# Performance work log

Hardware: AMD Instinct MI355X
Metric: run time of the kernel (lower is better)

## Reference

```python
import jax, jax.numpy as jnp
import numpy as np

B, S, H, A, F, NCATE, VOCAB, EMB, NCONT = 64, 1024, 512, 256, 2048, 4, 1000, 64, 4


def _layernorm(x, g, b, eps=1e-5):
    m = jnp.mean(x, axis=-1, keepdims=True)
    v = jnp.mean((x - m) ** 2, axis=-1, keepdims=True)
    return (x - m) * jax.lax.rsqrt(v + eps) * g + b


def _positional_encoding(seq_len, d, base=10000.0):
    pos = jnp.arange(seq_len, dtype=jnp.float32)[:, None]
    i = jnp.arange(0, d, 2, dtype=jnp.float32)[None, :]
    ang = pos / jnp.power(base, i / d)
    pe = jnp.zeros((seq_len, d), dtype=jnp.float32)
    pe = pe.at[:, 0::2].set(jnp.sin(ang))
    pe = pe.at[:, 1::2].set(jnp.cos(ang))
    return pe


def setup_inputs() -> dict:
    key = jax.random.key(0)
    ks = jax.random.split(key, 24)
    s = lambda i, shape, fan: jax.random.normal(ks[i], shape, jnp.float32) / np.sqrt(fan)
    inp = {
        'cate_x': jax.random.randint(ks[0], (B, S, NCATE), 0, VOCAB, jnp.int32),
        'cont_x': jax.random.normal(ks[1], (B, S, NCONT), jnp.float32),
        'mask': (jax.random.uniform(ks[2], (B, S)) < 0.9).astype(jnp.float32),
        'targets': jax.random.uniform(ks[3], (B, S), jnp.float32),
        'E_cate': s(4, (NCATE, VOCAB, EMB), EMB),
        'W_proj': s(5, (NCATE * EMB + NCONT, H), NCATE * EMB + NCONT),
        'WQ1': s(6, (H, A), H), 'WK1': s(7, (H, A), H), 'WV1': s(8, (H, A), H),
        'WQ2': s(9, (H, A), H), 'WK2': s(10, (H, A), H), 'WV2': s(11, (H, A), H),
        'W0': s(12, (2 * A, H), 2 * A),
        'ln1_g': jnp.ones((H,), jnp.float32), 'ln1_b': jnp.zeros((H,), jnp.float32),
        'Wf1': s(13, (H, F), H), 'bf1': jnp.zeros((F,), jnp.float32),
        'Wf2': s(14, (F, H), F), 'bf2': jnp.zeros((H,), jnp.float32),
        'ln2_g': jnp.ones((H,), jnp.float32), 'ln2_b': jnp.zeros((H,), jnp.float32),
        'Wfin': s(15, (H, 1), H), 'bfin': jnp.zeros((1,), jnp.float32),
    }
    return inp


def _attn_branch(x, WQ, WK, WV, mask_bias):
    Q = x @ WQ  # [B,S,A]
    K = x @ WK
    V = x @ WV
    scores = jnp.einsum('bsa,bta->bst', Q, K) / np.sqrt(A)
    scores = scores + mask_bias  # additive key-mask [B,1,S]
    return jnp.einsum('bst,bta->bsa', jax.nn.softmax(scores, axis=-1), V)


def reference(cate_x, cont_x, mask, targets, E_cate, W_proj, WQ1, WK1, WV1,
              WQ2, WK2, WV2, W0, ln1_g, ln1_b, Wf1, bf1, Wf2, bf2, ln2_g,
              ln2_b, Wfin, bfin):
    # embedding: per-feature lookup, concat with continuous, project to hidden
    emb = jax.vmap(lambda tab, idx: tab[idx], in_axes=(0, 2), out_axes=2)(E_cate, cate_x)
    emb = emb.reshape(B, S, NCATE * EMB)
    x = jnp.concatenate([emb, cont_x], axis=-1) @ W_proj  # [B,S,H]
    x = x + _positional_encoding(S, H)[None]
    mask_bias = (mask * 1e6 - 1e6)[:, None, :]  # [B,1,S]
    z1 = _attn_branch(x, WQ1, WK1, WV1, mask_bias)
    z2 = _attn_branch(x, WQ2, WK2, WV2, mask_bias)
    z = jnp.concatenate([z1, z2], axis=-1) @ W0
    z = _layernorm(x + z, ln1_g, ln1_b)
    fz = jax.nn.relu(z @ Wf1 + bf1) @ Wf2 + bf2
    z3 = _layernorm(z + fz, ln2_g, ln2_b)
    out = (z3 @ Wfin + bfin).squeeze(-1)  # [B,S]
    return out
```

## Files before the change

kernel.cpp:

```cpp
#include <hip/hip_runtime.h>

typedef unsigned short ushort_t;
typedef unsigned int uint32;
typedef float f32x4 __attribute__((ext_vector_type(4)));
typedef short bf16x8 __attribute__((ext_vector_type(8)));

__device__ __forceinline__ float bf2f(short u) {
  union { uint32 u32; float f; } cv;
  cv.u32 = ((uint32)(ushort_t)u) << 16;
  return cv.f;
}
__device__ __forceinline__ ushort_t f2bf(float f) {
  union { float f; uint32 u; } cv; cv.f = f;
  return (ushort_t)((cv.u + 0x7fffu + ((cv.u >> 16) & 1u)) >> 16);
}
__device__ __forceinline__ uint32 pack2bf(float lo, float hi) {
  return (uint32)f2bf(lo) | ((uint32)f2bf(hi) << 16);
}
__device__ __forceinline__ f32x4 mfma16(bf16x8 a, bf16x8 b, f32x4 c) {
  return __builtin_amdgcn_mfma_f32_16x16x32_bf16(a, b, c, 0, 0, 0);
}
__device__ __forceinline__ void gld_lds16(const ushort_t* g, ushort_t* l) {
  __builtin_amdgcn_global_load_lds(
      (const __attribute__((address_space(1))) void*)g,
      (__attribute__((address_space(3))) void*)l, 16, 0, 0);
}

struct TPtrs {
  const float* s[9];
  ushort_t* d[9];
};
__global__ __launch_bounds__(256)
void transpose_all(TPtrs p) {
  const int id = blockIdx.x;
  const float* S;
  ushort_t* D;
  int K, N, lt;
  if (id < 768) {
    const int wsel = id >> 7;
    lt = id & 127; S = p.s[wsel]; D = p.d[wsel]; K = 512; N = 256;
  } else if (id < 1024) {
    lt = id - 768; S = p.s[6]; D = p.d[6]; K = 512; N = 512;
  } else if (id < 2048) {
    lt = id - 1024; S = p.s[7]; D = p.d[7]; K = 512; N = 2048;
  } else {
    lt = id - 2048; S = p.s[8]; D = p.d[8]; K = 2048; N = 512;
  }
  const int ntn = N >> 5;
  const int k0 = (lt / ntn) * 32, n0 = (lt % ntn) * 32;
  __shared__ float sm[32][33];
  const int tx = threadIdx.x & 31, ty = threadIdx.x >> 5;
#pragma unroll
  for (int i = 0; i < 4; ++i)
    sm[ty + i * 8][tx] = S[(size_t)(k0 + ty + i * 8) * N + n0 + tx];
  __syncthreads();
#pragma unroll
  for (int i = 0; i < 4; ++i)
    D[(size_t)(n0 + ty + i * 8) * K + k0 + tx] = f2bf(sm[tx][ty + i * 8]);
}

__global__ __launch_bounds__(256)
void ep_kernel(const float* __restrict__ E, const float* __restrict__ Wp,
               ushort_t* __restrict__ EP) {
  const int cv = blockIdx.x;
  const int c = cv / 1000;
  __shared__ float se[64];
  if (threadIdx.x < 64) se[threadIdx.x] = E[(size_t)cv * 64 + threadIdx.x];
  __syncthreads();
  const float* wrow = Wp + (size_t)c * 64 * 512;
  for (int h = threadIdx.x; h < 512; h += 256) {
    float acc = 0.f;
#pragma unroll
    for (int e = 0; e < 64; ++e) acc += se[e] * wrow[(size_t)e * 512 + h];
    EP[(size_t)cv * 512 + h] = f2bf(acc);
  }
}

__global__ __launch_bounds__(256)
void pe_kernel(float* __restrict__ PE) {
  const int id = blockIdx.x * 256 + threadIdx.x;
  const int s = id >> 8, i = id & 255;
  const float ang = (float)s * exp2f(-(float)i * (13.287712379549449f / 256.0f));
  PE[(size_t)s * 512 + 2 * i] = sinf(ang);
  PE[(size_t)s * 512 + 2 * i + 1] = cosf(ang);
}

__global__ __launch_bounds__(256)
void x_kernel(const int* __restrict__ cate, const float* __restrict__ cont,
              const float* __restrict__ Wp, const ushort_t* __restrict__ EP,
              const float* __restrict__ PE, ushort_t* __restrict__ X) {
  const int tid = threadIdx.x;
  const size_t r = (size_t)blockIdx.x * 4 + (tid >> 6);
  const int lane = tid & 63;
  const int h0 = lane * 8;
  const int s = (int)(r & 1023);
  float acc[8];
  const float4 p0 = *(const float4*)(PE + (size_t)s * 512 + h0);
  const float4 p1 = *(const float4*)(PE + (size_t)s * 512 + h0 + 4);
  acc[0] = p0.x; acc[1] = p0.y; acc[2] = p0.z; acc[3] = p0.w;
  acc[4] = p1.x; acc[5] = p1.y; acc[6] = p1.z; acc[7] = p1.w;
#pragma unroll
  for (int c = 0; c < 4; ++c) {
    const int idx = cate[r * 4 + c];
    const bf16x8 e8 = *(const bf16x8*)(EP + ((size_t)(c * 1000 + idx)) * 512 + h0);
#pragma unroll
    for (int k = 0; k < 8; ++k) acc[k] += bf2f(e8[k]);
  }
#pragma unroll
  for (int j = 0; j < 4; ++j) {
    const float cj = cont[r * 4 + j];
    const float4 w0 = *(const float4*)(Wp + (size_t)(256 + j) * 512 + h0);
    const float4 w1 = *(const float4*)(Wp + (size_t)(256 + j) * 512 + h0 + 4);
    acc[0] += cj * w0.x; acc[1] += cj * w0.y; acc[2] += cj * w0.z; acc[3] += cj * w0.w;
    acc[4] += cj * w1.x; acc[5] += cj * w1.y; acc[6] += cj * w1.z; acc[7] += cj * w1.w;
  }
  bf16x8 ov;
#pragma unroll
  for (int k = 0; k < 8; ++k) ov[k] = (short)f2bf(acc[k]);
  *(bf16x8*)(X + r * 512 + h0) = ov;
}

template <int EPI, bool TSTORE>
__global__ __launch_bounds__(256, 3)
void gemm_bt(const ushort_t* __restrict__ A, const ushort_t* __restrict__ BT,
             ushort_t* __restrict__ C, const float* __restrict__ bias, int N, int K) {
  __shared__ __align__(16) ushort_t sA[128 * 64];
  __shared__ __align__(16) ushort_t sB[128 * 64];
  const int tid = threadIdx.x;
  const int lane = tid & 63;
  const int wid = tid >> 6;
  const int l15 = lane & 15, l4 = lane >> 4;
  const int wr = (wid >> 1) * 64, wc = (wid & 1) * 64;
  const size_t rowA0 = (size_t)blockIdx.x * 128;
  const size_t rowB0 = (size_t)blockIdx.y * 128;

  f32x4 acc[4][4] = {};

  for (int kt = 0; kt < K; kt += 64) {
#pragma unroll
    for (int it = 0; it < 4; ++it) {
      const int L = it * 256 + tid;
      const int row = L >> 3;
      const int c = (L & 7) ^ (row & 7);
      gld_lds16(A + (rowA0 + row) * K + kt + c * 8, sA + (size_t)L * 8);
      gld_lds16(BT + (rowB0 + row) * K + kt + c * 8, sB + (size_t)L * 8);
    }
    __syncthreads();
#pragma unroll
    for (int kk = 0; kk < 2; ++kk) {
      bf16x8 af[4], bfr[4];
#pragma unroll
      for (int mi = 0; mi < 4; ++mi) {
        const int row = wr + mi * 16 + l15;
        const int c = (kk * 4 + l4) ^ (row & 7);
        af[mi] = *(const bf16x8*)(sA + row * 64 + c * 8);
      }
#pragma unroll
      for (int ni = 0; ni < 4; ++ni) {
        const int row = wc + ni * 16 + l15;
        const int c = (kk * 4 + l4) ^ (row & 7);
        bfr[ni] = *(const bf16x8*)(sB + row * 64 + c * 8);
      }
#pragma unroll
      for (int mi = 0; mi < 4; ++mi)
#pragma unroll
        for (int ni = 0; ni < 4; ++ni)
          acc[mi][ni] = mfma16(af[mi], bfr[ni], acc[mi][ni]);
    }
    __syncthreads();
  }
#pragma unroll
  for (int ni = 0; ni < 4; ++ni) {
    const int col = (int)rowB0 + wc + ni * 16 + l15;
    float bv = 0.f;
    if (EPI > 0) bv = bias[col];
#pragma unroll
    for (int mi = 0; mi < 4; ++mi) {
      const size_t row0 = rowA0 + wr + mi * 16 + l4 * 4;
      if (TSTORE) {
        ushort4 ov;
        ov.x = f2bf(acc[mi][ni][0]);
        ov.y = f2bf(acc[mi][ni][1]);
        ov.z = f2bf(acc[mi][ni][2]);
        ov.w = f2bf(acc[mi][ni][3]);
        *(ushort4*)(C + ((row0 >> 10) * 256 + (size_t)col) * 1024 + (row0 & 1023)) = ov;
      } else {
#pragma unroll
        for (int j = 0; j < 4; ++j) {
          float v = acc[mi][ni][j] + bv;
          if (EPI == 2) v = fmaxf(v, 0.f);
          C[(row0 + j) * N + col] = f2bf(v);
        }
      }
    }
  }
}

__global__ __launch_bounds__(256, 2)
void attn_kernel(const ushort_t* __restrict__ Q, const ushort_t* __restrict__ Kb,
                 const ushort_t* __restrict__ VT, const float* __restrict__ mask,
                 ushort_t* __restrict__ Z, int colOff) {
  __shared__ __align__(16) ushort_t sK[64 * 256];
  __shared__ __align__(16) ushort_t sV[256 * 64];
  const int tid = threadIdx.x, lane = tid & 63, w = tid >> 6;
  const int l15 = lane & 15, l4 = lane >> 4;
  const int id = blockIdx.x;
  const int b = ((id >> 7) << 3) | (id & 7);
  const int qb = (id >> 3) & 15;
  const int q0 = qb * 64 + w * 16;

  bf16x8 qf[8];
  {
    const ushort_t* qrow = Q + ((size_t)b * 1024 + q0 + l15) * 256;
#pragma unroll
    for (int kk = 0; kk < 8; ++kk)
      qf[kk] = *(const bf16x8*)(qrow + kk * 32 + l4 * 8);
  }
  float m_run = -3.0e38f, l_run = 0.f;
  f32x4 o[16] = {};
  const int src0 = ((l4 & 1) << 5) + l15;
  const bool hiSel = (l4 >= 2);

  for (int t0 = 0; t0 < 1024; t0 += 64) {
#pragma unroll
    for (int it = 0; it < 8; ++it) {
      const int L = it * 256 + tid;
      const int rk = L >> 5;
      const int ck = (L & 24) | ((L ^ rk) & 7);
      gld_lds16(Kb + ((size_t)b * 1024 + t0 + rk) * 256 + ck * 8, sK + (size_t)L * 8);
      const int rv = L >> 3;
      const int cv2 = (L ^ rv) & 7;
      gld_lds16(VT + ((size_t)b * 256 + rv) * 1024 + t0 + cv2 * 8, sV + (size_t)L * 8);
    }
    __syncthreads();

    __builtin_amdgcn_s_setprio(1);
    f32x4 st[4] = {};
#pragma unroll
    for (int fi = 0; fi < 4; ++fi) {
      const int row = fi * 16 + l15;
      const ushort_t* kr = sK + row * 256;
#pragma unroll
      for (int kk = 0; kk < 8; ++kk) {
        const int c = kk * 4 + l4;
        const int cs = (c & 24) | ((c ^ row) & 7);
        const bf16x8 kf = *(const bf16x8*)(kr + cs * 8);
        st[fi] = mfma16(kf, qf[kk], st[fi]);
      }
    }
    __builtin_amdgcn_s_setprio(0);

    float pr[4][4];
    float tmax = -3.0e38f;
#pragma unroll
    for (int fi = 0; fi < 4; ++fi) {
      const float4 mk = *(const float4*)(mask + (size_t)b * 1024 + t0 + fi * 16 + l4 * 4);
      pr[fi][0] = st[fi][0] * 0.0625f + (mk.x * 1e6f - 1e6f);
      pr[fi][1] = st[fi][1] * 0.0625f + (mk.y * 1e6f - 1e6f);
      pr[fi][2] = st[fi][2] * 0.0625f + (mk.z * 1e6f - 1e6f);
      pr[fi][3] = st[fi][3] * 0.0625f + (mk.w * 1e6f - 1e6f);
      tmax = fmaxf(tmax, fmaxf(fmaxf(pr[fi][0], pr[fi][1]), fmaxf(pr[fi][2], pr[fi][3])));
    }
    tmax = fmaxf(tmax, __shfl_xor(tmax, 16));
    tmax = fmaxf(tmax, __shfl_xor(tmax, 32));

    if (!__all(tmax <= m_run + 8.f)) {
      const float m_new = fmaxf(m_run, tmax);
      const float alpha = __expf(m_run - m_new);
      l_run *= alpha;
      m_run = m_new;
#pragma unroll
      for (int ai = 0; ai < 16; ++ai) o[ai] *= alpha;
    }

    float rs = 0.f;
#pragma unroll
    for (int fi = 0; fi < 4; ++fi)
#pragma unroll
      for (int j = 0; j < 4; ++j) {
        pr[fi][j] = __expf(pr[fi][j] - m_run);
        rs += pr[fi][j];
      }
    rs += __shfl_xor(rs, 16);
    rs += __shfl_xor(rs, 32);
    l_run += rs;

    uint32 pk[4][2];
#pragma unroll
    for (int fi = 0; fi < 4; ++fi) {
      pk[fi][0] = pack2bf(pr[fi][0], pr[fi][1]);
      pk[fi][1] = pack2bf(pr[fi][2], pr[fi][3]);
    }
    bf16x8 pf[2];
#pragma unroll
    for (int kk2 = 0; kk2 < 2; ++kk2) {
      const uint32 a0 = __shfl(pk[2 * kk2][0], src0);
      const uint32 a1 = __shfl(pk[2 * kk2][1], src0);
      const uint32 a2 = __shfl(pk[2 * kk2][0], src0 + 16);
      const uint32 a3 = __shfl(pk[2 * kk2][1], src0 + 16);
      const uint32 b0 = __shfl(pk[2 * kk2 + 1][0], src0);
      const uint32 b1 = __shfl(pk[2 * kk2 + 1][1], src0);
      const uint32 b2 = __shfl(pk[2 * kk2 + 1][0], src0 + 16);
      const uint32 b3 = __shfl(pk[2 * kk2 + 1][1], src0 + 16);
      uint4 wv;
      wv.x = hiSel ? b0 : a0;
      wv.y = hiSel ? b1 : a1;
      wv.z = hiSel ? b2 : a2;
      wv.w = hiSel ? b3 : a3;
      pf[kk2] = __builtin_bit_cast(bf16x8, wv);
    }

    __builtin_amdgcn_s_setprio(1);
#pragma unroll
    for (int ai = 0; ai < 16; ++ai) {
      const int row = ai * 16 + l15;
      const ushort_t* vr = sV + row * 64;
#pragma unroll
      for (int kk2 = 0; kk2 < 2; ++kk2) {
        const int c = (kk2 * 4 + l4) ^ (row & 7);
        const bf16x8 vf = *(const bf16x8*)(vr + c * 8);
        o[ai] = mfma16(vf, pf[kk2], o[ai]);
      }
    }
    __builtin_amdgcn_s_setprio(0);
    __syncthreads();
  }

  const float inv = 1.f / l_run;
  const size_t zrow = ((size_t)b * 1024 + q0 + l15) * 512;
#pragma unroll
  for (int ai = 0; ai < 16; ++ai) {
    ushort4 ov;
    ov.x = f2bf(o[ai][0] * inv);
    ov.y = f2bf(o[ai][1] * inv);
    ov.z = f2bf(o[ai][2] * inv);
    ov.w = f2bf(o[ai][3] * inv);
    *(ushort4*)(Z + zrow + colOff + ai * 16 + l4 * 4) = ov;
  }
}

__global__ __launch_bounds__(256)
void ln_kernel(const ushort_t* __restrict__ Xa, const ushort_t* __restrict__ Xb2,
               const float* __restrict__ g, const float* __restrict__ bb,
               ushort_t* __restrict__ O) {
  const int tid = threadIdx.x;
  const size_t r = (size_t)blockIdx.x * 4 + (tid >> 6);
  const int lane = tid & 63;
  const int h0 = lane * 8;
  const bf16x8 va = *(const bf16x8*)(Xa + r * 512 + h0);
  const bf16x8 vb = *(const bf16x8*)(Xb2 + r * 512 + h0);
  float v[8], s1 = 0.f, s2 = 0.f;
#pragma unroll
  for (int k = 0; k < 8; ++k) {
    v[k] = bf2f(va[k]) + bf2f(vb[k]);
    s1 += v[k];
    s2 += v[k] * v[k];
  }
#pragma unroll
  for (int m = 1; m < 64; m <<= 1) {
    s1 += __shfl_xor(s1, m);
    s2 += __shfl_xor(s2, m);
  }
  const float mean = s1 * (1.f / 512.f);
  const float var = s2 * (1.f / 512.f) - mean * mean;
  const float rstd = rsqrtf(var + 1e-5f);
  const float4 g0 = *(const float4*)(g + h0);
  const float4 g1 = *(const float4*)(g + h0 + 4);
  const float4 b0 = *(const float4*)(bb + h0);
  const float4 b1 = *(const float4*)(bb + h0 + 4);
  const float gg[8] = {g0.x, g0.y, g0.z, g0.w, g1.x, g1.y, g1.z, g1.w};
  const float bbv[8] = {b0.x, b0.y, b0.z, b0.w, b1.x, b1.y, b1.z, b1.w};
  bf16x8 ov;
#pragma unroll
  for (int k = 0; k < 8; ++k)
    ov[k] = (short)f2bf((v[k] - mean) * rstd * gg[k] + bbv[k]);
  *(bf16x8*)(O + r * 512 + h0) = ov;
}

__global__ __launch_bounds__(256)
void ln_fin_kernel(const ushort_t* __restrict__ Xa, const ushort_t* __restrict__ Xb2,
                   const float* __restrict__ g, const float* __restrict__ bb,
                   const float* __restrict__ Wfin, const float* __restrict__ bfin,
                   float* __restrict__ out) {
  const int tid = threadIdx.x;
  const size_t r = (size_t)blockIdx.x * 4 + (tid >> 6);
  const int lane = tid & 63;
  const int h0 = lane * 8;
  const bf16x8 va = *(const bf16x8*)(Xa + r * 512 + h0);
  const bf16x8 vb = *(const bf16x8*)(Xb2 + r * 512 + h0);
  float v[8], s1 = 0.f, s2 = 0.f;
#pragma unroll
  for (int k = 0; k < 8; ++k) {
    v[k] = bf2f(va[k]) + bf2f(vb[k]);
    s1 += v[k];
    s2 += v[k] * v[k];
  }
#pragma unroll
  for (int m = 1; m < 64; m <<= 1) {
    s1 += __shfl_xor(s1, m);
    s2 += __shfl_xor(s2, m);
  }
  const float mean = s1 * (1.f / 512.f);
  const float var = s2 * (1.f / 512.f) - mean * mean;
  const float rstd = rsqrtf(var + 1e-5f);
  const float4 g0 = *(const float4*)(g + h0);
  const float4 g1 = *(const float4*)(g + h0 + 4);
  const float4 b0 = *(const float4*)(bb + h0);
  const float4 b1 = *(const float4*)(bb + h0 + 4);
  const float4 w0 = *(const float4*)(Wfin + h0);
  const float4 w1 = *(const float4*)(Wfin + h0 + 4);
  const float gg[8] = {g0.x, g0.y, g0.z, g0.w, g1.x, g1.y, g1.z, g1.w};
  const float bbv[8] = {b0.x, b0.y, b0.z, b0.w, b1.x, b1.y, b1.z, b1.w};
  const float ww[8] = {w0.x, w0.y, w0.z, w0.w, w1.x, w1.y, w1.z, w1.w};
  float dot = 0.f;
#pragma unroll
  for (int k = 0; k < 8; ++k)
    dot += ((v[k] - mean) * rstd * gg[k] + bbv[k]) * ww[k];
#pragma unroll
  for (int m = 1; m < 64; m <<= 1) dot += __shfl_xor(dot, m);
  if (lane == 0) out[r] = dot + bfin[0];
}

extern "C" void kernel_launch(void* const* d_in, const int* in_sizes, int n_in,
                              void* d_out, int out_size, void* d_ws, size_t ws_size,
                              hipStream_t stream) {
  (void)in_sizes; (void)n_in; (void)out_size; (void)ws_size;
  const int* cate   = (const int*)d_in[0];
  const float* cont = (const float*)d_in[1];
  const float* mask = (const float*)d_in[2];
  const float* E    = (const float*)d_in[4];
  const float* Wp   = (const float*)d_in[5];
  const float* WQ1  = (const float*)d_in[6];
  const float* WK1  = (const float*)d_in[7];
  const float* WV1  = (const float*)d_in[8];
  const float* WQ2  = (const float*)d_in[9];
  const float* WK2  = (const float*)d_in[10];
  const float* WV2  = (const float*)d_in[11];
  const float* W0   = (const float*)d_in[12];
  const float* ln1g = (const float*)d_in[13];
  const float* ln1b = (const float*)d_in[14];
  const float* Wf1  = (const float*)d_in[15];
  const float* bf1  = (const float*)d_in[16];
  const float* Wf2  = (const float*)d_in[17];
  const float* bf2  = (const float*)d_in[18];
  const float* ln2g = (const float*)d_in[19];
  const float* ln2b = (const float*)d_in[20];
  const float* Wfin = (const float*)d_in[21];
  const float* bfin = (const float*)d_in[22];
  float* out = (float*)d_out;
  char* ws = (char*)d_ws;

  const size_t MB = 1ull << 20;
  ushort_t* Xb  = (ushort_t*)(ws + 0);
  ushort_t* Qb  = (ushort_t*)(ws + 64 * MB);
  ushort_t* Kb  = (ushort_t*)(ws + 96 * MB);
  ushort_t* VTb = (ushort_t*)(ws + 128 * MB);
  ushort_t* Zb  = (ushort_t*)(ws + 160 * MB);
  ushort_t* T0b = (ushort_t*)(ws + 64 * MB);
  ushort_t* H1b = (ushort_t*)(ws + 128 * MB);
  ushort_t* Gb  = (ushort_t*)(ws + 0);
  ushort_t* T1b = (ushort_t*)(ws + 64 * MB);
  const size_t OW = 224 * MB;
  ushort_t* wq1t = (ushort_t*)(ws + OW + 0);
  ushort_t* wk1t = (ushort_t*)(ws + OW + 262144);
  ushort_t* wv1t = (ushort_t*)(ws + OW + 524288);
  ushort_t* wq2t = (ushort_t*)(ws + OW + 786432);
  ushort_t* wk2t = (ushort_t*)(ws + OW + 1048576);
  ushort_t* wv2t = (ushort_t*)(ws + OW + 1310720);
  ushort_t* w0t  = (ushort_t*)(ws + OW + 1572864);
  ushort_t* wf1t = (ushort_t*)(ws + OW + 2097152);
  ushort_t* wf2t = (ushort_t*)(ws + OW + 4194304);
  ushort_t* epb  = (ushort_t*)(ws + OW + 6291456);
  float*    peb  = (float*)   (ws + OW + 10485760);

  const dim3 blk(256);
  TPtrs tp;
  tp.s[0] = WQ1; tp.s[1] = WK1; tp.s[2] = WV1;
  tp.s[3] = WQ2; tp.s[4] = WK2; tp.s[5] = WV2;
  tp.s[6] = W0;  tp.s[7] = Wf1; tp.s[8] = Wf2;
  tp.d[0] = wq1t; tp.d[1] = wk1t; tp.d[2] = wv1t;
  tp.d[3] = wq2t; tp.d[4] = wk2t; tp.d[5] = wv2t;
  tp.d[6] = w0t;  tp.d[7] = wf1t; tp.d[8] = wf2t;
  transpose_all<<<dim3(3072), blk, 0, stream>>>(tp);
  ep_kernel<<<4000, blk, 0, stream>>>(E, Wp, epb);
  pe_kernel<<<1024, blk, 0, stream>>>(peb);
  x_kernel<<<16384, blk, 0, stream>>>(cate, cont, Wp, epb, peb, Xb);
  gemm_bt<0, false><<<dim3(512, 2), blk, 0, stream>>>(Xb, wq1t, Qb, nullptr, 256, 512);
  gemm_bt<0, false><<<dim3(512, 2), blk, 0, stream>>>(Xb, wk1t, Kb, nullptr, 256, 512);
  gemm_bt<0, true><<<dim3(512, 2), blk, 0, stream>>>(Xb, wv1t, VTb, nullptr, 256, 512);
  attn_kernel<<<dim3(1024), blk, 0, stream>>>(Qb, Kb, VTb, mask, Zb, 0);
  gemm_bt<0, false><<<dim3(512, 2), blk, 0, stream>>>(Xb, wq2t, Qb, nullptr, 256, 512);
  gemm_bt<0, false><<<dim3(512, 2), blk, 0, stream>>>(Xb, wk2t, Kb, nullptr, 256, 512);
  gemm_bt<0, true><<<dim3(512, 2), blk, 0, stream>>>(Xb, wv2t, VTb, nullptr, 256, 512);
  attn_kernel<<<dim3(1024), blk, 0, stream>>>(Qb, Kb, VTb, mask, Zb, 256);
  gemm_bt<0, false><<<dim3(512, 4), blk, 0, stream>>>(Zb, w0t, T0b, nullptr, 512, 512);
  ln_kernel<<<16384, blk, 0, stream>>>(Xb, T0b, ln1g, ln1b, H1b);
  for (int rc = 0; rc < 4; ++rc) {
    const ushort_t* h1c = H1b + (size_t)rc * 16384 * 512;
    ushort_t* t1c = T1b + (size_t)rc * 16384 * 512;
    gemm_bt<2, false><<<dim3(128, 16), blk, 0, stream>>>(h1c, wf1t, Gb, bf1, 2048, 512);
    gemm_bt<1, false><<<dim3(128, 4), blk, 0, stream>>>(Gb, wf2t, t1c, bf2, 512, 2048);
  }
  ln_fin_kernel<<<16384, blk, 0, stream>>>(H1b, T1b, ln2g, ln2b, Wfin, bfin, out);
}
```

Measured before the change: 994.0 us.

## Fuse Q/K/V projections into one GEMM and widen attention blocks to 8 waves

```diff
diff --git a/kernel.cpp b/kernel.cpp
--- a/kernel.cpp
+++ b/kernel.cpp
@@ -196,7 +196,81 @@
   }
 }
 
-__global__ __launch_bounds__(256, 2)
+__global__ __launch_bounds__(256, 3)
+void gemm_qkv(const ushort_t* __restrict__ A, const ushort_t* __restrict__ BT,
+              ushort_t* __restrict__ Qo, ushort_t* __restrict__ Ko,
+              ushort_t* __restrict__ VTo) {
+  __shared__ __align__(16) ushort_t sA[128 * 64];
+  __shared__ __align__(16) ushort_t sB[128 * 64];
+  const int tid = threadIdx.x;
+  const int lane = tid & 63;
+  const int wid = tid >> 6;
+  const int l15 = lane & 15, l4 = lane >> 4;
+  const int wr = (wid >> 1) * 64, wc = (wid & 1) * 64;
+  const size_t rowA0 = (size_t)blockIdx.x * 128;
+  const size_t rowB0 = (size_t)blockIdx.y * 128;
+  const int K = 512;
+
+  f32x4 acc[4][4] = {};
+
+  for (int kt = 0; kt < K; kt += 64) {
+#pragma unroll
+    for (int it = 0; it < 4; ++it) {
+      const int L = it * 256 + tid;
+      const int row = L >> 3;
+      const int c = (L & 7) ^ (row & 7);
+      gld_lds16(A + (rowA0 + row) * K + kt + c * 8, sA + (size_t)L * 8);
+      gld_lds16(BT + (rowB0 + row) * K + kt + c * 8, sB + (size_t)L * 8);
+    }
+    __syncthreads();
+#pragma unroll
+    for (int kk = 0; kk < 2; ++kk) {
+      bf16x8 af[4], bfr[4];
+#pragma unroll
+      for (int mi = 0; mi < 4; ++mi) {
+        const int row = wr + mi * 16 + l15;
+        const int c = (kk * 4 + l4) ^ (row & 7);
+        af[mi] = *(const bf16x8*)(sA + row * 64 + c * 8);
+      }
+#pragma unroll
+      for (int ni = 0; ni < 4; ++ni) {
+        const int row = wc + ni * 16 + l15;
+        const int c = (kk * 4 + l4) ^ (row & 7);
+        bfr[ni] = *(const bf16x8*)(sB + row * 64 + c * 8);
+      }
+#pragma unroll
+      for (int mi = 0; mi < 4; ++mi)
+#pragma unroll
+        for (int ni = 0; ni < 4; ++ni)
+          acc[mi][ni] = mfma16(af[mi], bfr[ni], acc[mi][ni]);
+    }
+    __syncthreads();
+  }
+  const int sel = (int)blockIdx.y >> 1;
+#pragma unroll
+  for (int ni = 0; ni < 4; ++ni) {
+    const int colL = ((int)blockIdx.y & 1) * 128 + wc + ni * 16 + l15;
+#pragma unroll
+    for (int mi = 0; mi < 4; ++mi) {
+      const size_t row0 = rowA0 + wr + mi * 16 + l4 * 4;
+      if (sel == 2) {
+        ushort4 ov;
+        ov.x = f2bf(acc[mi][ni][0]);
+        ov.y = f2bf(acc[mi][ni][1]);
+        ov.z = f2bf(acc[mi][ni][2]);
+        ov.w = f2bf(acc[mi][ni][3]);
+        *(ushort4*)(VTo + ((row0 >> 10) * 256 + (size_t)colL) * 1024 + (row0 & 1023)) = ov;
+      } else {
+        ushort_t* O = sel ? Ko : Qo;
+#pragma unroll
+        for (int j = 0; j < 4; ++j)
+          O[(row0 + j) * 256 + colL] = f2bf(acc[mi][ni][j]);
+      }
+    }
+  }
+}
+
+__global__ __launch_bounds__(512, 2)
 void attn_kernel(const ushort_t* __restrict__ Q, const ushort_t* __restrict__ Kb,
                  const ushort_t* __restrict__ VT, const float* __restrict__ mask,
                  ushort_t* __restrict__ Z, int colOff) {
@@ -205,9 +279,9 @@
   const int tid = threadIdx.x, lane = tid & 63, w = tid >> 6;
   const int l15 = lane & 15, l4 = lane >> 4;
   const int id = blockIdx.x;
-  const int b = ((id >> 7) << 3) | (id & 7);
-  const int qb = (id >> 3) & 15;
-  const int q0 = qb * 64 + w * 16;
+  const int b = ((id >> 6) << 3) | (id & 7);
+  const int qb = (id >> 3) & 7;
+  const int q0 = qb * 128 + w * 16;
 
   bf16x8 qf[8];
   {
@@ -223,8 +297,8 @@
 
   for (int t0 = 0; t0 < 1024; t0 += 64) {
 #pragma unroll
-    for (int it = 0; it < 8; ++it) {
-      const int L = it * 256 + tid;
+    for (int it = 0; it < 4; ++it) {
+      const int L = it * 512 + tid;
       const int rk = L >> 5;
       const int ck = (L & 24) | ((L ^ rk) & 7);
       gld_lds16(Kb + ((size_t)b * 1024 + t0 + rk) * 256 + ck * 8, sK + (size_t)L * 8);
@@ -234,7 +308,6 @@
     }
     __syncthreads();
 
-    __builtin_amdgcn_s_setprio(1);
     f32x4 st[4] = {};
 #pragma unroll
     for (int fi = 0; fi < 4; ++fi) {
@@ -248,7 +321,6 @@
         st[fi] = mfma16(kf, qf[kk], st[fi]);
       }
     }
-    __builtin_amdgcn_s_setprio(0);
 
     float pr[4][4];
     float tmax = -3.0e38f;
@@ -310,7 +382,6 @@
       pf[kk2] = __builtin_bit_cast(bf16x8, wv);
     }
 
-    __builtin_amdgcn_s_setprio(1);
 #pragma unroll
     for (int ai = 0; ai < 16; ++ai) {
       const int row = ai * 16 + l15;
@@ -322,7 +393,6 @@
         o[ai] = mfma16(vf, pf[kk2], o[ai]);
       }
     }
-    __builtin_amdgcn_s_setprio(0);
     __syncthreads();
   }
 
@@ -485,14 +555,10 @@
   ep_kernel<<<4000, blk, 0, stream>>>(E, Wp, epb);
   pe_kernel<<<1024, blk, 0, stream>>>(peb);
   x_kernel<<<16384, blk, 0, stream>>>(cate, cont, Wp, epb, peb, Xb);
-  gemm_bt<0, false><<<dim3(512, 2), blk, 0, stream>>>(Xb, wq1t, Qb, nullptr, 256, 512);
-  gemm_bt<0, false><<<dim3(512, 2), blk, 0, stream>>>(Xb, wk1t, Kb, nullptr, 256, 512);
-  gemm_bt<0, true><<<dim3(512, 2), blk, 0, stream>>>(Xb, wv1t, VTb, nullptr, 256, 512);
-  attn_kernel<<<dim3(1024), blk, 0, stream>>>(Qb, Kb, VTb, mask, Zb, 0);
-  gemm_bt<0, false><<<dim3(512, 2), blk, 0, stream>>>(Xb, wq2t, Qb, nullptr, 256, 512);
-  gemm_bt<0, false><<<dim3(512, 2), blk, 0, stream>>>(Xb, wk2t, Kb, nullptr, 256, 512);
-  gemm_bt<0, true><<<dim3(512, 2), blk, 0, stream>>>(Xb, wv2t, VTb, nullptr, 256, 512);
-  attn_kernel<<<dim3(1024), blk, 0, stream>>>(Qb, Kb, VTb, mask, Zb, 256);
+  gemm_qkv<<<dim3(512, 6), blk, 0, stream>>>(Xb, wq1t, Qb, Kb, VTb);
+  attn_kernel<<<dim3(512), dim3(512), 0, stream>>>(Qb, Kb, VTb, mask, Zb, 0);
+  gemm_qkv<<<dim3(512, 6), blk, 0, stream>>>(Xb, wq2t, Qb, Kb, VTb);
+  attn_kernel<<<dim3(512), dim3(512), 0, stream>>>(Qb, Kb, VTb, mask, Zb, 256);
   gemm_bt<0, false><<<dim3(512, 4), blk, 0, stream>>>(Zb, w0t, T0b, nullptr, 512, 512);
   ln_kernel<<<16384, blk, 0, stream>>>(Xb, T0b, ln1g, ln1b, H1b);
   for (int rc = 0; rc < 4; ++rc) {
```

Result: slower. 1.087 ms (+9.4%).
